# Optimization experiments

Measured on AMD Instinct MI355X. Metric: run time of the kernel, lower is better.

Reference implementation:

```python
import jax, jax.numpy as jnp
import numpy as np

N_GRAPHS = 100
BN_EPS = 1e-5
L = 4


def batch_norm(x, gamma, beta):
    # torch BatchNorm1d in training mode: biased batch statistics over the node dim
    mu = jnp.mean(x, axis=0)
    var = jnp.var(x, axis=0)
    return gamma * (x - mu) * jax.lax.rsqrt(var + BN_EPS) + beta


def setup_inputs() -> dict:
    key = jax.random.key(0)
    ks = jax.random.split(key, 24)
    N, E, IN, H, C = 50000, 600000, 128, 128, 10
    s = 0.05
    inp = {
        "h": jax.random.normal(ks[0], (N, IN), jnp.float32),
        "snorm_n": jax.random.uniform(ks[1], (N, 1), jnp.float32),
        "edge_src": jax.random.randint(ks[2], (E,), 0, N, jnp.int32),
        "edge_dst": jax.random.randint(ks[3], (E,), 0, N, jnp.int32),
        "graph_ids": jnp.sort(jax.random.randint(ks[4], (N,), 0, N_GRAPHS, jnp.int32)),
        # embedding_h
        "emb_W": jax.random.normal(ks[5], (IN, H), jnp.float32) * s,
        "emb_b": jnp.zeros((H,), jnp.float32),
        # per-layer GIN params, stacked over L layers
        "eps": jnp.zeros((L,), jnp.float32),
        "W1": jax.random.normal(ks[6], (L, H, H), jnp.float32) * s,
        "b1": jnp.zeros((L, H), jnp.float32),
        "g1": jnp.ones((L, H), jnp.float32),   # MLP internal BN gamma
        "be1": jnp.zeros((L, H), jnp.float32),  # MLP internal BN beta
        "W2": jax.random.normal(ks[7], (L, H, H), jnp.float32) * s,
        "b2": jnp.zeros((L, H), jnp.float32),
        "ga": jnp.ones((L, H), jnp.float32),    # ApplyNodeFunc BN gamma
        "ba": jnp.zeros((L, H), jnp.float32),
        "gl": jnp.ones((L, H), jnp.float32),    # GINLayer node BN gamma
        "bl": jnp.zeros((L, H), jnp.float32),
        # linears_prediction (L+1 of them)
        "pred_W": jax.random.normal(ks[8], (L + 1, H, C), jnp.float32) * s,
        "pred_b": jnp.zeros((L + 1, C), jnp.float32),
    }
    return inp


def reference(h, snorm_n, edge_src, edge_dst, graph_ids, emb_W, emb_b, eps,
              W1, b1, g1, be1, W2, b2, ga, ba, gl, bl, pred_W, pred_b):
    N = h.shape[0]
    h = h @ emb_W + emb_b  # embedding_h
    hidden_rep = [h]
    for i in range(L):
        h_in = h
        # sum-aggregate neighbor features (irregular gather + scatter-add)
        neigh = jax.ops.segment_sum(h[edge_src], edge_dst, num_segments=N)
        z = (1.0 + eps[i]) * h + neigh
        # ApplyNodeFunc: MLP (lin->BN->relu->lin) then BN then relu
        z = jax.nn.relu(batch_norm(z @ W1[i] + b1[i], g1[i], be1[i]))
        z = z @ W2[i] + b2[i]
        z = jax.nn.relu(batch_norm(z, ga[i], ba[i]))
        z = z * snorm_n                      # graph_norm
        z = batch_norm(z, gl[i], bl[i])      # batch_norm
        z = jax.nn.relu(z)
        h = h_in + z                         # residual (dropout p=0)
        hidden_rep.append(h)
    score = jnp.zeros((N_GRAPHS, pred_W.shape[-1]), h.dtype)
    for i, hr in enumerate(hidden_rep):
        pooled = jax.ops.segment_sum(hr, graph_ids, num_segments=N_GRAPHS)
        score = score + pooled @ pred_W[i] + pred_b[i]
    return score
```

## Files before the change

kernel.cpp:

```cpp
#include <hip/hip_runtime.h>

#define HD __device__ __forceinline__

static constexpr int H = 128;
static constexpr int G = 100;
static constexpr int L = 4;
static constexpr int C = 10;
static constexpr int DEGCAP = 64;
static constexpr int CNT_PAD = 50048;

typedef __attribute__((ext_vector_type(8))) short short8;
typedef __attribute__((ext_vector_type(4))) float f32x4;

HD float bf2f(unsigned int u16) {
    return __uint_as_float(u16 << 16);
}
HD unsigned int f2bf(float f) {
    unsigned int u = __float_as_uint(f);
    u += 0x7fffu + ((u >> 16) & 1u);
    return u >> 16;
}

__global__ __launch_bounds__(256) void prep_kernel(
    const float* __restrict__ embW, const float* __restrict__ W1, const float* __restrict__ W2,
    unsigned short* __restrict__ WT, unsigned short* __restrict__ Hb,
    const int* __restrict__ src, const int* __restrict__ dst, int E,
    int* __restrict__ cnt, int* __restrict__ esrc) {
    int b = blockIdx.x;
    if (b < 576) {
        int mat = b >> 6;
        int bx = b & 63;
        if (b == 0 && threadIdx.x < 64)
            ((unsigned int*)Hb)[threadIdx.x] = 0u;
        const float* s = (mat == 0) ? embW
                       : (mat <= L) ? W1 + (size_t)(mat - 1) * H * H
                                    : W2 + (size_t)(mat - 1 - L) * H * H;
        int t = bx * 256 + threadIdx.x;
        int col = t >> 7, k = t & 127;
        WT[(size_t)mat * H * H + col * H + k] = (unsigned short)f2bf(s[(size_t)k * H + col]);
    } else {
        int e = (b - 576) * 256 + threadIdx.x;
        if (e < E) {
            int d = dst[e];
            int pos = atomicAdd(&cnt[d], 1) & (DEGCAP - 1);
            esrc[(size_t)d * DEGCAP + pos] = src[e] + 1;
        }
    }
}

__global__ __launch_bounds__(1024, 2) void aggemm_kernel(
    const unsigned short* __restrict__ HbZ, const int* __restrict__ cnt,
    const int* __restrict__ esrc, const float* __restrict__ eps, int layer,
    const unsigned short* __restrict__ WT, const float* __restrict__ bias,
    unsigned short* __restrict__ outB, int N,
    float* __restrict__ sum_out, float* __restrict__ sq_out) {
    __shared__ unsigned short As[64 * 136];
    int tid = threadIdx.x;
    int w = tid >> 6, lane = tid & 63, q = lane >> 4, m = lane & 15;
    int row0 = blockIdx.x * 64;

    {
        const unsigned int* H2 = (const unsigned int*)HbZ;
        float e1 = 1.0f + eps[layer];
#pragma unroll
        for (int i = 0; i < 4; ++i) {
            int r = w * 4 + i;
            int node = row0 + r;
            unsigned int out = 0;
            if (node < N) {
                unsigned int hv = H2[(size_t)(node + 1) * 64 + lane];
                float ax = e1 * bf2f(hv & 0xffffu);
                float ay = e1 * bf2f(hv >> 16);
                int deg = min(cnt[node], DEGCAP);
                int degPad = min((deg + 15) & ~15, DEGCAP);
                const int* ep = esrc + (size_t)node * DEGCAP;
                for (int j = 0; j < degPad; j += 16) {
                    unsigned int v[16];
#pragma unroll
                    for (int u = 0; u < 16; ++u) v[u] = H2[(size_t)ep[j + u] * 64 + lane];
                    float sx[4] = {0.f, 0.f, 0.f, 0.f}, sy[4] = {0.f, 0.f, 0.f, 0.f};
#pragma unroll
                    for (int u = 0; u < 16; ++u) {
                        sx[u & 3] += bf2f(v[u] & 0xffffu);
                        sy[u & 3] += bf2f(v[u] >> 16);
                    }
                    ax += (sx[0] + sx[1]) + (sx[2] + sx[3]);
                    ay += (sy[0] + sy[1]) + (sy[2] + sy[3]);
                }
                out = f2bf(ax) | (f2bf(ay) << 16);
            }
            *(unsigned int*)&As[r * 136 + lane * 2] = out;
        }
    }
    __syncthreads();

    int mrow = (w >> 2) * 16;
    int colbase = (w & 3) * 32;
    short8 bfrag[2][4];
#pragma unroll
    for (int nt = 0; nt < 2; ++nt) {
        const unsigned short* wc = WT + (size_t)(colbase + nt * 16 + m) * H;
#pragma unroll
        for (int kk = 0; kk < 4; ++kk)
            bfrag[nt][kk] = *(const short8*)&wc[kk * 32 + q * 8];
    }
    f32x4 acc[2] = {(f32x4){0.f, 0.f, 0.f, 0.f}, (f32x4){0.f, 0.f, 0.f, 0.f}};
#pragma unroll
    for (int kk = 0; kk < 4; ++kk) {
        short8 af = *(const short8*)&As[(mrow + m) * 136 + kk * 32 + q * 8];
#pragma unroll
        for (int nt = 0; nt < 2; ++nt)
            acc[nt] = __builtin_amdgcn_mfma_f32_16x16x32_bf16(af, bfrag[nt][kk], acc[nt], 0, 0, 0);
    }

    float bs2[2] = {bias[colbase + m], bias[colbase + 16 + m]};
    float s[2] = {0.f, 0.f}, qq[2] = {0.f, 0.f};
#pragma unroll
    for (int nt = 0; nt < 2; ++nt) {
        int gcol = colbase + nt * 16 + m;
#pragma unroll
        for (int rg = 0; rg < 4; ++rg) {
            int grow = row0 + mrow + q * 4 + rg;
            float v = acc[nt][rg] + bs2[nt];
            if (grow < N) {
                outB[(size_t)grow * H + gcol] = (unsigned short)f2bf(v);
                s[nt] += v;
                qq[nt] += v * v;
            }
        }
    }
#pragma unroll
    for (int nt = 0; nt < 2; ++nt) {
        s[nt] += __shfl_xor(s[nt], 16); s[nt] += __shfl_xor(s[nt], 32);
        qq[nt] += __shfl_xor(qq[nt], 16); qq[nt] += __shfl_xor(qq[nt], 32);
    }
    __syncthreads();
    float* SS = (float*)As;
    float* QQ = SS + 4 * H;
    if (q == 0) {
#pragma unroll
        for (int nt = 0; nt < 2; ++nt) {
            int col = colbase + nt * 16 + m;
            SS[(w >> 2) * H + col] = s[nt];
            QQ[(w >> 2) * H + col] = qq[nt];
        }
    }
    __syncthreads();
    if (tid < H) {
        atomicAdd(&sum_out[tid], SS[tid] + SS[H + tid] + SS[2 * H + tid] + SS[3 * H + tid]);
        atomicAdd(&sq_out[tid], QQ[tid] + QQ[H + tid] + QQ[2 * H + tid] + QQ[3 * H + tid]);
    }
}

template <bool ABF16, bool TRANS, bool STATS, bool POOLF, bool HOFF>
__global__ __launch_bounds__(256, 4) void mgemm_kernel(
    const float* __restrict__ Af, const unsigned short* __restrict__ Ab,
    const unsigned short* __restrict__ WT, const float* __restrict__ bias,
    const float* __restrict__ sum_in, const float* __restrict__ sq_in,
    const float* __restrict__ gam, const float* __restrict__ bet, float invN,
    unsigned short* __restrict__ outB,
    int N, float* __restrict__ sum_out, float* __restrict__ sq_out,
    const int* __restrict__ gids, float* __restrict__ pool) {
    __shared__ unsigned short As[64 * 136];
    __shared__ float cas[H], ccs[H];
    int tid = threadIdx.x;
    int w = tid >> 6, lane = tid & 63, q = lane >> 4, m = lane & 15;
    int row0 = blockIdx.x * 64;
    int colbase = w * 32;

    short8 bfrag[2][4];
#pragma unroll
    for (int nt = 0; nt < 2; ++nt) {
        const unsigned short* wc = WT + (size_t)(colbase + nt * 16 + m) * H;
#pragma unroll
        for (int kk = 0; kk < 4; ++kk)
            bfrag[nt][kk] = *(const short8*)&wc[kk * 32 + q * 8];
    }

    if (TRANS) {
        if (tid < H) {
            float mu = sum_in[tid] * invN;
            float var = sq_in[tid] * invN - mu * mu;
            float inv = rsqrtf(var + 1e-5f);
            float a = gam[tid] * inv;
            cas[tid] = a;
            ccs[tid] = bet[tid] - mu * a;
        }
        __syncthreads();
    }

    {
        int cc = tid & 15, rg = tid >> 4;
        int c0 = cc * 8;
        float a8[8], b8[8];
        if (TRANS) {
#pragma unroll
            for (int j = 0; j < 8; ++j) { a8[j] = cas[c0 + j]; b8[j] = ccs[c0 + j]; }
        }
#pragma unroll
        for (int rr = 0; rr < 4; ++rr) {
            int r = rg * 4 + rr;
            int gr = row0 + r;
            uint4 o = {0u, 0u, 0u, 0u};
            if (ABF16 && !TRANS) {
                if (gr < N) o = *(const uint4*)&Ab[(size_t)gr * H + c0];
            } else {
                float v[8] = {0.f, 0.f, 0.f, 0.f, 0.f, 0.f, 0.f, 0.f};
                if (gr < N) {
                    if (ABF16) {
                        uint4 x = *(const uint4*)&Ab[(size_t)gr * H + c0];
                        v[0] = bf2f(x.x & 0xffffu); v[1] = bf2f(x.x >> 16);
                        v[2] = bf2f(x.y & 0xffffu); v[3] = bf2f(x.y >> 16);
                        v[4] = bf2f(x.z & 0xffffu); v[5] = bf2f(x.z >> 16);
                        v[6] = bf2f(x.w & 0xffffu); v[7] = bf2f(x.w >> 16);
                    } else {
                        float4 x0 = *(const float4*)&Af[(size_t)gr * H + c0];
                        float4 x1 = *(const float4*)&Af[(size_t)gr * H + c0 + 4];
                        v[0] = x0.x; v[1] = x0.y; v[2] = x0.z; v[3] = x0.w;
                        v[4] = x1.x; v[5] = x1.y; v[6] = x1.z; v[7] = x1.w;
                    }
                }
                if (TRANS) {
#pragma unroll
                    for (int j = 0; j < 8; ++j) v[j] = fmaxf(a8[j] * v[j] + b8[j], 0.f);
                }
                o.x = f2bf(v[0]) | (f2bf(v[1]) << 16);
                o.y = f2bf(v[2]) | (f2bf(v[3]) << 16);
                o.z = f2bf(v[4]) | (f2bf(v[5]) << 16);
                o.w = f2bf(v[6]) | (f2bf(v[7]) << 16);
            }
            *(uint4*)&As[r * 136 + c0] = o;
        }
    }
    __syncthreads();

    f32x4 acc[4][2];
#pragma unroll
    for (int mt = 0; mt < 4; ++mt)
#pragma unroll
        for (int nt = 0; nt < 2; ++nt) acc[mt][nt] = (f32x4){0.f, 0.f, 0.f, 0.f};
#pragma unroll
    for (int kk = 0; kk < 4; ++kk) {
        short8 af[4];
#pragma unroll
        for (int mt = 0; mt < 4; ++mt)
            af[mt] = *(const short8*)&As[(mt * 16 + m) * 136 + kk * 32 + q * 8];
#pragma unroll
        for (int mt = 0; mt < 4; ++mt)
#pragma unroll
            for (int nt = 0; nt < 2; ++nt)
                acc[mt][nt] = __builtin_amdgcn_mfma_f32_16x16x32_bf16(
                    af[mt], bfrag[nt][kk], acc[mt][nt], 0, 0, 0);
    }

    float bs2[2] = {bias[colbase + m], bias[colbase + 16 + m]};
    float s[2] = {0.f, 0.f}, qq[2] = {0.f, 0.f};
#pragma unroll
    for (int mt = 0; mt < 4; ++mt)
#pragma unroll
        for (int nt = 0; nt < 2; ++nt) {
            int gcol = colbase + nt * 16 + m;
#pragma unroll
            for (int rg = 0; rg < 4; ++rg) {
                int grow = row0 + mt * 16 + q * 4 + rg;
                float v = acc[mt][nt][rg] + bs2[nt];
                if (grow < N) {
                    outB[(size_t)(HOFF ? grow + 1 : grow) * H + gcol] = (unsigned short)f2bf(v);
                    if (STATS || POOLF) {
                        s[nt] += v;
                        if (STATS) qq[nt] += v * v;
                    }
                }
            }
        }

    if (STATS) {
#pragma unroll
        for (int nt = 0; nt < 2; ++nt) {
            float sv = s[nt], qv = qq[nt];
            sv += __shfl_xor(sv, 16); sv += __shfl_xor(sv, 32);
            qv += __shfl_xor(qv, 16); qv += __shfl_xor(qv, 32);
            if (q == 0) {
                atomicAdd(&sum_out[colbase + nt * 16 + m], sv);
                atomicAdd(&sq_out[colbase + nt * 16 + m], qv);
            }
        }
    }

    if (POOLF) {
        int last = min(row0 + 63, N - 1);
        bool uni = (gids[row0] == gids[last]);
        if (uni) {
            int g = gids[row0];
#pragma unroll
            for (int nt = 0; nt < 2; ++nt) {
                float sv = s[nt];
                sv += __shfl_xor(sv, 16); sv += __shfl_xor(sv, 32);
                if (q == 0) atomicAdd(&pool[g * H + colbase + nt * 16 + m], sv);
            }
        } else {
#pragma unroll
            for (int mt = 0; mt < 4; ++mt)
#pragma unroll
                for (int nt = 0; nt < 2; ++nt)
#pragma unroll
                    for (int rg = 0; rg < 4; ++rg) {
                        int grow = row0 + mt * 16 + q * 4 + rg;
                        if (grow < N) {
                            float v = acc[mt][nt][rg] + bs2[nt];
                            atomicAdd(&pool[gids[grow] * H + colbase + nt * 16 + m], v);
                        }
                    }
        }
    }
}

__global__ __launch_bounds__(256) void statsv_kernel(const unsigned short* __restrict__ UB,
                                                     const float* __restrict__ snorm,
                                                     const float* __restrict__ sum2, const float* __restrict__ sq2,
                                                     const float* __restrict__ ga, const float* __restrict__ ba,
                                                     float invN, int N,
                                                     float* __restrict__ sum3, float* __restrict__ sq3) {
    __shared__ float cas[H], ccs[H];
    int t = threadIdx.x;
    if (t < H) {
        float m = sum2[t] * invN;
        float var = sq2[t] * invN - m * m;
        float inv = rsqrtf(var + 1e-5f);
        float a = ga[t] * inv;
        cas[t] = a;
        ccs[t] = ba[t] - m * a;
    }
    __syncthreads();
    int col2 = t & 63, part = t >> 6;
    int c0 = col2 * 2, c1 = c0 + 1;
    float a0 = cas[c0], b0 = ccs[c0], a1 = cas[c1], b1 = ccs[c1];
    float s0 = 0.f, q0 = 0.f, s1 = 0.f, q1 = 0.f;
    const unsigned int* U2 = (const unsigned int*)UB;
    for (int r = blockIdx.x * 4 + part; r < N; r += gridDim.x * 4) {
        float sn = snorm[r];
        unsigned int v = U2[(size_t)r * 64 + col2];
        float v0 = fmaxf(a0 * bf2f(v & 0xffffu) + b0, 0.f) * sn;
        float v1 = fmaxf(a1 * bf2f(v >> 16) + b1, 0.f) * sn;
        s0 += v0; q0 += v0 * v0;
        s1 += v1; q1 += v1 * v1;
    }
    __shared__ float S[4][H], Q[4][H];
    S[part][c0] = s0; S[part][c1] = s1;
    Q[part][c0] = q0; Q[part][c1] = q1;
    __syncthreads();
    if (t < H) {
        atomicAdd(&sum3[t], S[0][t] + S[1][t] + S[2][t] + S[3][t]);
        atomicAdd(&sq3[t], Q[0][t] + Q[1][t] + Q[2][t] + Q[3][t]);
    }
}

__global__ __launch_bounds__(256) void tail_kernel(unsigned short* __restrict__ HbZ,
                                                   const unsigned short* __restrict__ UB,
                                                   const float* __restrict__ snorm,
                                                   const float* __restrict__ sum2, const float* __restrict__ sq2,
                                                   const float* __restrict__ ga, const float* __restrict__ ba,
                                                   const float* __restrict__ sum3, const float* __restrict__ sq3,
                                                   const float* __restrict__ gl, const float* __restrict__ bl,
                                                   float invN, const int* __restrict__ gids,
                                                   float* __restrict__ pool, int N) {
    __shared__ float ca2[H], cc2[H], ca3[H], cc3[H];
    __shared__ float PS[8][H];
    int t = threadIdx.x;
    if (t < H) {
        float m2 = sum2[t] * invN, v2 = sq2[t] * invN - m2 * m2;
        float i2 = rsqrtf(v2 + 1e-5f), a2 = ga[t] * i2;
        ca2[t] = a2; cc2[t] = ba[t] - m2 * a2;
        float m3 = sum3[t] * invN, v3 = sq3[t] * invN - m3 * m3;
        float i3 = rsqrtf(v3 + 1e-5f), a3 = gl[t] * i3;
        ca3[t] = a3; cc3[t] = bl[t] - m3 * a3;
    }
    __syncthreads();
    int row0 = blockIdx.x * 32;
    int col4 = t & 31, rowg = t >> 5;
    int c0 = col4 * 4;
    float A2[4], B2[4], A3[4], B3[4];
#pragma unroll
    for (int j = 0; j < 4; ++j) {
        A2[j] = ca2[c0 + j]; B2[j] = cc2[c0 + j];
        A3[j] = ca3[c0 + j]; B3[j] = cc3[c0 + j];
    }
    bool uni = (gids[row0] == gids[min(row0 + 31, N - 1)]);
    float p[4] = {0.f, 0.f, 0.f, 0.f};
    const uint2* U4 = (const uint2*)UB;
    uint2* H4 = (uint2*)HbZ;
#pragma unroll
    for (int rr = 0; rr < 4; ++rr) {
        int r = row0 + rowg * 4 + rr;
        if (r < N) {
            float sn = snorm[r];
            uint2 uv = U4[(size_t)r * 32 + col4];
            uint2 hv = H4[(size_t)(r + 1) * 32 + col4];
            float u[4] = {bf2f(uv.x & 0xffffu), bf2f(uv.x >> 16), bf2f(uv.y & 0xffffu), bf2f(uv.y >> 16)};
            float h[4] = {bf2f(hv.x & 0xffffu), bf2f(hv.x >> 16), bf2f(hv.y & 0xffffu), bf2f(hv.y >> 16)};
#pragma unroll
            for (int j = 0; j < 4; ++j) {
                float v = fmaxf(A2[j] * u[j] + B2[j], 0.f) * sn;
                h[j] += fmaxf(A3[j] * v + B3[j], 0.f);
            }
            uint2 hb;
            hb.x = f2bf(h[0]) | (f2bf(h[1]) << 16);
            hb.y = f2bf(h[2]) | (f2bf(h[3]) << 16);
            H4[(size_t)(r + 1) * 32 + col4] = hb;
            if (uni) {
                p[0] += h[0]; p[1] += h[1]; p[2] += h[2]; p[3] += h[3];
            } else {
                int g = gids[r];
#pragma unroll
                for (int j = 0; j < 4; ++j) atomicAdd(&pool[g * H + c0 + j], h[j]);
            }
        }
    }
    if (uni) {
#pragma unroll
        for (int j = 0; j < 4; ++j) PS[rowg][c0 + j] = p[j];
        __syncthreads();
        if (t < H) {
            float s = PS[0][t] + PS[1][t] + PS[2][t] + PS[3][t] +
                      PS[4][t] + PS[5][t] + PS[6][t] + PS[7][t];
            atomicAdd(&pool[gids[row0] * H + t], s);
        }
    }
}

__global__ __launch_bounds__(128) void final_kernel(const float* __restrict__ pool,
                                                    const float* __restrict__ pw,
                                                    const float* __restrict__ pb,
                                                    float* __restrict__ out) {
    int g = blockIdx.x, t = threadIdx.x;
    float acc[C];
#pragma unroll
    for (int c = 0; c < C; ++c) acc[c] = 0.f;
#pragma unroll
    for (int i = 0; i <= L; ++i) {
        float p = pool[(size_t)(i * G + g) * H + t];
        const float* wrow = pw + (size_t)(i * H + t) * C;
#pragma unroll
        for (int c = 0; c < C; ++c) acc[c] += p * wrow[c];
    }
#pragma unroll
    for (int c = 0; c < C; ++c) {
        float v = acc[c];
        v += __shfl_xor(v, 1);  v += __shfl_xor(v, 2);  v += __shfl_xor(v, 4);
        v += __shfl_xor(v, 8);  v += __shfl_xor(v, 16); v += __shfl_xor(v, 32);
        acc[c] = v;
    }
    __shared__ float Ws[2][C];
    if ((t & 63) == 0) {
        int wv = t >> 6;
#pragma unroll
        for (int c = 0; c < C; ++c) Ws[wv][c] = acc[c];
    }
    __syncthreads();
    if (t < C) {
        float s = Ws[0][t] + Ws[1][t];
#pragma unroll
        for (int i = 0; i <= L; ++i) s += pb[i * C + t];
        out[g * C + t] = s;
    }
}

extern "C" void kernel_launch(void* const* d_in, const int* in_sizes, int n_in,
                              void* d_out, int out_size, void* d_ws, size_t ws_size,
                              hipStream_t stream) {
    const float* h_in  = (const float*)d_in[0];
    const float* snorm = (const float*)d_in[1];
    const int* esrc_in = (const int*)d_in[2];
    const int* edst_in = (const int*)d_in[3];
    const int* gids    = (const int*)d_in[4];
    const float* embW = (const float*)d_in[5];
    const float* embB = (const float*)d_in[6];
    const float* eps  = (const float*)d_in[7];
    const float* W1   = (const float*)d_in[8];
    const float* b1   = (const float*)d_in[9];
    const float* g1   = (const float*)d_in[10];
    const float* be1  = (const float*)d_in[11];
    const float* W2   = (const float*)d_in[12];
    const float* b2   = (const float*)d_in[13];
    const float* ga   = (const float*)d_in[14];
    const float* ba   = (const float*)d_in[15];
    const float* gl   = (const float*)d_in[16];
    const float* bl   = (const float*)d_in[17];
    const float* predW = (const float*)d_in[18];
    const float* predB = (const float*)d_in[19];

    const int N = in_sizes[0] / H;
    const int E = in_sizes[2];
    const float invN = 1.0f / (float)N;

    float* ws = (float*)d_ws;
    float* POOL = ws;
    float* STATS = POOL + (size_t)(L + 1) * G * H;
    int* CNT = (int*)(STATS + (size_t)L * 6 * H);
    int* ESRC = CNT + CNT_PAD;
    unsigned short* WT = (unsigned short*)(ESRC + (size_t)N * DEGCAP);
    unsigned short* Hb = WT + (size_t)9 * H * H;
    unsigned short* ZB = Hb + (size_t)(N + 1) * H;
    unsigned short* TB = ZB + (size_t)N * H;
    unsigned short* UB = ZB;

    size_t zbytes = ((size_t)(L + 1) * G * H + (size_t)L * 6 * H + CNT_PAD + (size_t)N * DEGCAP) * 4;
    hipMemsetAsync(POOL, 0, zbytes, stream);

    int prep_blocks = 576 + (E + 255) / 256;
    prep_kernel<<<prep_blocks, 256, 0, stream>>>(embW, W1, W2, WT, Hb,
                                                 esrc_in, edst_in, E, CNT, ESRC);

    int gblocks = (N + 63) / 64;
    mgemm_kernel<false, false, false, true, true><<<gblocks, 256, 0, stream>>>(
        h_in, nullptr, WT, embB, nullptr, nullptr, nullptr, nullptr, invN,
        Hb, N, nullptr, nullptr, gids, POOL);

    for (int i = 0; i < L; ++i) {
        float* S1 = STATS + (size_t)i * 6 * H;
        float* Q1 = S1 + H;
        float* S2 = Q1 + H;
        float* Q2 = S2 + H;
        float* S3 = Q2 + H;
        float* Q3 = S3 + H;
        aggemm_kernel<<<gblocks, 1024, 0, stream>>>(
            Hb, CNT, ESRC, eps, i, WT + (size_t)(1 + i) * H * H, b1 + (size_t)i * H,
            TB, N, S1, Q1);
        mgemm_kernel<true, true, true, false, false><<<gblocks, 256, 0, stream>>>(
            nullptr, TB, WT + (size_t)(1 + L + i) * H * H, b2 + (size_t)i * H,
            S1, Q1, g1 + (size_t)i * H, be1 + (size_t)i * H, invN,
            UB, N, S2, Q2, nullptr, nullptr);
        statsv_kernel<<<256, 256, 0, stream>>>(UB, snorm, S2, Q2,
                                               ga + (size_t)i * H, ba + (size_t)i * H, invN, N, S3, Q3);
        tail_kernel<<<(N + 31) / 32, 256, 0, stream>>>(Hb, UB, snorm,
                                                       S2, Q2, ga + (size_t)i * H, ba + (size_t)i * H,
                                                       S3, Q3, gl + (size_t)i * H, bl + (size_t)i * H,
                                                       invN, gids, POOL + (size_t)(i + 1) * G * H, N);
    }
    final_kernel<<<G, 128, 0, stream>>>(POOL, predW, predB, (float*)d_out);
}
```

Measured before the change: 633.2 us.

## Software-pipeline neighbor gathers via global_load_lds double-buffered staging

```diff
diff --git a/kernel.cpp b/kernel.cpp
--- a/kernel.cpp
+++ b/kernel.cpp
@@ -19,6 +19,12 @@
     unsigned int u = __float_as_uint(f);
     u += 0x7fffu + ((u >> 16) & 1u);
     return u >> 16;
+}
+
+HD void gll(const unsigned int* src, unsigned int* ldsdst) {
+    __builtin_amdgcn_global_load_lds(
+        (const __attribute__((address_space(1))) unsigned int*)src,
+        (__attribute__((address_space(3))) unsigned int*)ldsdst, 4, 0, 0);
 }
 
 __global__ __launch_bounds__(256) void prep_kernel(
@@ -55,6 +61,8 @@
     unsigned short* __restrict__ outB, int N,
     float* __restrict__ sum_out, float* __restrict__ sq_out) {
     __shared__ unsigned short As[64 * 136];
+    __shared__ unsigned int stage[16][2][256];
+    __shared__ int eplds[16][64];
     int tid = threadIdx.x;
     int w = tid >> 6, lane = tid & 63, q = lane >> 4, m = lane & 15;
     int row0 = blockIdx.x * 64;
@@ -62,34 +70,85 @@
     {
         const unsigned int* H2 = (const unsigned int*)HbZ;
         float e1 = 1.0f + eps[layer];
-#pragma unroll
-        for (int i = 0; i < 4; ++i) {
-            int r = w * 4 + i;
-            int node = row0 + r;
-            unsigned int out = 0;
-            if (node < N) {
-                unsigned int hv = H2[(size_t)(node + 1) * 64 + lane];
-                float ax = e1 * bf2f(hv & 0xffffu);
-                float ay = e1 * bf2f(hv >> 16);
-                int deg = min(cnt[node], DEGCAP);
-                int degPad = min((deg + 15) & ~15, DEGCAP);
-                const int* ep = esrc + (size_t)node * DEGCAP;
-                for (int j = 0; j < degPad; j += 16) {
+        int nb = row0 + w * 4;
+        unsigned int* stA = &stage[w][0][0];
+        unsigned int* stB = &stage[w][1][0];
+        int* epw = &eplds[w][0];
+
+        {
+            int n = lane >> 4, u = lane & 15;
+            int nd = min(nb + n, N - 1);
+            gll((const unsigned int*)(esrc + (size_t)nd * DEGCAP + u), (unsigned int*)epw);
+        }
+        int deg[4]; unsigned int self[4];
+#pragma unroll
+        for (int n = 0; n < 4; ++n) {
+            int nd = nb + n;
+            deg[n] = (nd < N) ? min(cnt[nd], DEGCAP) : 0;
+            self[n] = (nd < N) ? H2[(size_t)(nd + 1) * 64 + lane] : 0u;
+        }
+        asm volatile("s_waitcnt vmcnt(0)" ::: "memory");
+
+        float acc[4][2];
+#pragma unroll
+        for (int n = 0; n < 4; ++n) {
+            acc[n][0] = e1 * bf2f(self[n] & 0xffffu);
+            acc[n][1] = e1 * bf2f(self[n] >> 16);
+        }
+
+        int4 idx = *(const int4*)&epw[0];
+        int4 nidx;
+#pragma unroll
+        for (int c = 0; c < 16; ++c) {
+            if (c < 15) nidx = *(const int4*)&epw[(c + 1) * 4];
+            unsigned int* dst = (c & 1) ? stB : stA;
+            gll(H2 + (size_t)idx.x * 64 + lane, dst);
+            gll(H2 + (size_t)idx.y * 64 + lane, dst + 64);
+            gll(H2 + (size_t)idx.z * 64 + lane, dst + 128);
+            gll(H2 + (size_t)idx.w * 64 + lane, dst + 192);
+            if (c > 0) {
+                asm volatile("s_waitcnt vmcnt(4)" ::: "memory");
+                const unsigned int* sb = ((c - 1) & 1) ? stB : stA;
+                int n = (c - 1) >> 2;
+#pragma unroll
+                for (int k = 0; k < 4; ++k) {
+                    unsigned int v = sb[k * 64 + lane];
+                    acc[n][0] += bf2f(v & 0xffffu);
+                    acc[n][1] += bf2f(v >> 16);
+                }
+            }
+            idx = nidx;
+        }
+        asm volatile("s_waitcnt vmcnt(0)" ::: "memory");
+#pragma unroll
+        for (int k = 0; k < 4; ++k) {
+            unsigned int v = stB[k * 64 + lane];
+            acc[3][0] += bf2f(v & 0xffffu);
+            acc[3][1] += bf2f(v >> 16);
+        }
+
+#pragma unroll
+        for (int n = 0; n < 4; ++n) {
+            if (deg[n] > 16) {
+                const int* ep = esrc + (size_t)(nb + n) * DEGCAP;
+                int degPad = min((deg[n] + 15) & ~15, DEGCAP);
+                for (int j = 16; j < degPad; j += 16) {
                     unsigned int v[16];
 #pragma unroll
                     for (int u = 0; u < 16; ++u) v[u] = H2[(size_t)ep[j + u] * 64 + lane];
-                    float sx[4] = {0.f, 0.f, 0.f, 0.f}, sy[4] = {0.f, 0.f, 0.f, 0.f};
 #pragma unroll
                     for (int u = 0; u < 16; ++u) {
-                        sx[u & 3] += bf2f(v[u] & 0xffffu);
-                        sy[u & 3] += bf2f(v[u] >> 16);
+                        acc[n][0] += bf2f(v[u] & 0xffffu);
+                        acc[n][1] += bf2f(v[u] >> 16);
                     }
-                    ax += (sx[0] + sx[1]) + (sx[2] + sx[3]);
-                    ay += (sy[0] + sy[1]) + (sy[2] + sy[3]);
                 }
-                out = f2bf(ax) | (f2bf(ay) << 16);
-            }
-            *(unsigned int*)&As[r * 136 + lane * 2] = out;
+            }
+        }
+
+#pragma unroll
+        for (int n = 0; n < 4; ++n) {
+            unsigned int o = (nb + n < N) ? (f2bf(acc[n][0]) | (f2bf(acc[n][1]) << 16)) : 0u;
+            *(unsigned int*)&As[(w * 4 + n) * 136 + lane * 2] = o;
         }
     }
     __syncthreads();
```

After: 683.8 us. 8.0% more time.
